# Performance work log

Measured on AMD Instinct MI355X. Metric: run time of the kernel, lower is better.

Reference implementation:

```python
import jax, jax.numpy as jnp
import numpy as np

N, E = 50000, 800000          # nodes, edges (avg degree 16)
NFEAT, NHID, NCLASS = 256, 128, 64
HEADS = 4
P_DROP = 0.5


def setup_inputs() -> dict:
    key = jax.random.key(0)
    ks = jax.random.split(key, 12)

    def w(k, shape, fan_in):
        return jax.random.normal(k, shape, jnp.float32) * (1.0 / np.sqrt(fan_in))

    return {
        "features": jax.random.normal(ks[0], (N, NFEAT), jnp.float32),
        "src": jax.random.randint(ks[1], (E,), 0, N, jnp.int32),
        "dst": jax.random.randint(ks[2], (E,), 0, N, jnp.int32),
        # gc1: nfeat->nhid, 3 layers
        "wqkv1_0": w(ks[3], (3, NFEAT, NHID), NFEAT),
        "wqkv1_r": w(ks[4], (2, 3, NHID, NHID), NHID),
        "wo1": w(ks[5], (3, NHID, NHID), NHID),
        # gc2: nhid->nclass, 3 layers
        "wqkv2_0": w(ks[6], (3, NHID, NCLASS), NHID),
        "wqkv2_r": w(ks[7], (2, 3, NCLASS, NCLASS), NCLASS),
        "wo2": w(ks[8], (3, NCLASS, NCLASS), NCLASS),
        # gc3: nhid->nclass, 3 layers
        "wqkv3_0": w(ks[9], (3, NHID, NCLASS), NHID),
        "wqkv3_r": w(ks[10], (2, 3, NCLASS, NCLASS), NCLASS),
        "wo3": w(ks[11], (3, NCLASS, NCLASS), NCLASS),
    }


def _l2norm(x):
    # F.normalize(x): L2 along dim 1, eps=1e-12
    n = jnp.sqrt(jnp.sum(x * x, axis=1, keepdims=True))
    return x / jnp.maximum(n, 1e-12)


def _graph_transformer(h, src, dst, wqkv0, wqkvr, wo):
    """Stacked graph-transformer layers: gather q[dst]/k[src], edge-softmax per dst, scatter-sum v."""
    n = h.shape[0]
    n_layers = wo.shape[0]
    for l in range(n_layers):  # fixed small structural loop
        w = wqkv0 if l == 0 else wqkvr[l - 1]
        out_dim = w.shape[2]
        dh = out_dim // HEADS
        q = (h @ w[0]).reshape(n, HEADS, dh)
        k = (h @ w[1]).reshape(n, HEADS, dh)
        v = (h @ w[2]).reshape(n, HEADS, dh)
        # per-edge attention scores [E, H]
        s = jnp.einsum('ehd,ehd->eh', q[dst], k[src]) / np.sqrt(dh).astype(np.float32)
        # edge softmax over incoming edges of each dst node
        m = jax.ops.segment_max(s, dst, num_segments=n)
        e = jnp.exp(s - m[dst])
        denom = jax.ops.segment_sum(e, dst, num_segments=n)
        alpha = e / denom[dst]
        agg = jax.ops.segment_sum(alpha[:, :, None] * v[src], dst, num_segments=n)
        h = agg.reshape(n, out_dim) @ wo[l]
        if l < n_layers - 1:
            h = jax.nn.relu(h)
    return h


def reference(features, src, dst, wqkv1_0, wqkv1_r, wo1,
              wqkv2_0, wqkv2_r, wo2, wqkv3_0, wqkv3_r, wo3):
    key = jax.random.key(42)
    kd, ke = jax.random.split(key)

    x = _graph_transformer(features, src, dst, wqkv1_0, wqkv1_r, wo1)
    x = jax.nn.relu(_l2norm(x))
    # dropout (training=True), deterministic key
    keep = jax.random.bernoulli(kd, 1.0 - P_DROP, x.shape)
    x = jnp.where(keep, x / (1.0 - P_DROP), 0.0)

    mu = _l2norm(_graph_transformer(x, src, dst, wqkv2_0, wqkv2_r, wo2))
    logvar = _l2norm(_graph_transformer(x, src, dst, wqkv3_0, wqkv3_r, wo3))

    # reparameterize (training): std = exp(logvar) + 1e-12 (matches source exactly)
    std = jnp.exp(logvar) + 1e-12
    eps = jax.random.normal(ke, std.shape, std.dtype)
    z = eps * std + mu
    return z
```

## Files before the change

kernel.cpp:

```cpp
#include <hip/hip_runtime.h>
#include <stdint.h>
#include <math.h>

#define NN 50000
#define NE 800000
#define NH 4

typedef __attribute__((ext_vector_type(8))) short short8;
typedef __attribute__((ext_vector_type(4))) float floatx4;

__device__ inline float bf2f(uint32_t u16)
{
    return __uint_as_float(u16 << 16);
}
__device__ inline uint16_t f2bf(float f)
{
    uint32_t u = __float_as_uint(f);
    uint32_t r = (u + 0x7fffu + ((u >> 16) & 1u)) >> 16;
    return (uint16_t)r;
}
__device__ inline void unpk2(uint32_t w, float& lo, float& hi)
{
    lo = __uint_as_float(w << 16);
    hi = __uint_as_float(w & 0xffff0000u);
}
__device__ inline void unpk8(uint4 u, float* f)
{
    unpk2(u.x, f[0], f[1]);
    unpk2(u.y, f[2], f[3]);
    unpk2(u.z, f[4], f[5]);
    unpk2(u.w, f[6], f[7]);
}

__device__ inline void dot2bf(float& s, uint32_t a, uint32_t b)
{
    asm("v_dot2_f32_bf16 %0, %1, %2, %0" : "+v"(s) : "v"(a), "v"(b));
}

__device__ inline void wave_lds_sync()
{
    __builtin_amdgcn_wave_barrier();
    asm volatile("s_waitcnt lgkmcnt(0)" ::: "memory");
    __builtin_amdgcn_wave_barrier();
}

__host__ __device__ inline void tf2x32(uint32_t k0, uint32_t k1,
                                       uint32_t x0, uint32_t x1,
                                       uint32_t& o0, uint32_t& o1)
{
    uint32_t ks2 = k0 ^ k1 ^ 0x1BD11BDAu;
    x0 += k0; x1 += k1;
#define TF_R(r) { x0 += x1; x1 = (x1 << (r)) | (x1 >> (32 - (r))); x1 ^= x0; }
    TF_R(13) TF_R(15) TF_R(26) TF_R(6)
    x0 += k1;  x1 += ks2 + 1u;
    TF_R(17) TF_R(29) TF_R(16) TF_R(24)
    x0 += ks2; x1 += k0 + 2u;
    TF_R(13) TF_R(15) TF_R(26) TF_R(6)
    x0 += k0;  x1 += k1 + 3u;
    TF_R(17) TF_R(29) TF_R(16) TF_R(24)
    x0 += k1;  x1 += ks2 + 4u;
    TF_R(13) TF_R(15) TF_R(26) TF_R(6)
    x0 += ks2; x1 += k0 + 5u;
#undef TF_R
    o0 = x0; o1 = x1;
}

__device__ inline uint32_t jax_bits32(uint32_t k0, uint32_t k1, uint32_t idx)
{
    uint32_t a, b;
    tf2x32(k0, k1, 0u, idx, a, b);
    return a ^ b;
}

__device__ inline float jax_u01(uint32_t bits)
{
    return __uint_as_float((bits >> 9) | 0x3f800000u) - 1.0f;
}

__device__ inline float erfinv_f(float x)
{
    float w = -log1pf(-x * x);
    float p;
    if (w < 5.0f) {
        w = w - 2.5f;
        p = 2.81022636e-08f;
        p = fmaf(p, w, 3.43273939e-07f);
        p = fmaf(p, w, -3.5233877e-06f);
        p = fmaf(p, w, -4.39150654e-06f);
        p = fmaf(p, w, 0.00021858087f);
        p = fmaf(p, w, -0.00125372503f);
        p = fmaf(p, w, -0.00417768164f);
        p = fmaf(p, w, 0.246640727f);
        p = fmaf(p, w, 1.50140941f);
    } else {
        w = sqrtf(w) - 3.0f;
        p = -0.000200214257f;
        p = fmaf(p, w, 0.000100950558f);
        p = fmaf(p, w, 0.00134934322f);
        p = fmaf(p, w, -0.00367342844f);
        p = fmaf(p, w, 0.00573950773f);
        p = fmaf(p, w, -0.0076224613f);
        p = fmaf(p, w, 0.00943887047f);
        p = fmaf(p, w, 1.00167406f);
        p = fmaf(p, w, 2.83297682f);
    }
    return p * x;
}

__global__ __launch_bounds__(256) void fill_u32_k(uint32_t* p, uint32_t v, int n)
{
    int i = blockIdx.x * blockDim.x + threadIdx.x;
    if (i < n) p[i] = v;
}

struct WSeg { const float* src; int B, K, C, off; };
struct WSegs { WSeg s[18]; };

__global__ __launch_bounds__(256) void wconv_k(WSegs segs, uint16_t* __restrict__ Wt)
{
    WSeg sg = segs.s[blockIdx.y];
    int n = sg.B * sg.K * sg.C;
    int i = blockIdx.x * 256 + threadIdx.x;
    if (i >= n) return;
    int kc = sg.K * sg.C;
    int b = i / kc;
    int rr = i - b * kc;
    int k = rr / sg.C;
    int c = rr - k * sg.C;
    Wt[(size_t)sg.off + (size_t)(b * sg.C + c) * sg.K + k] = f2bf(sg.src[i]);
}

__global__ __launch_bounds__(256) void hist_k(const int* __restrict__ dst, int* __restrict__ deg)
{
    int e = blockIdx.x * blockDim.x + threadIdx.x;
    if (e < NE) atomicAdd(&deg[dst[e]], 1);
}

#define SCAN_CHUNK 1024
#define SCAN_NBLK  ((NN + SCAN_CHUNK - 1) / SCAN_CHUNK)

__global__ __launch_bounds__(256) void scan1_k(const int* __restrict__ deg,
                                               int* __restrict__ rowptr,
                                               int* __restrict__ bsums)
{
    __shared__ int lds[256];
    int b = blockIdx.x, t = threadIdx.x;
    int base = b * SCAN_CHUNK + t * 4;
    int v0 = (base + 0 < NN) ? deg[base + 0] : 0;
    int v1 = (base + 1 < NN) ? deg[base + 1] : 0;
    int v2 = (base + 2 < NN) ? deg[base + 2] : 0;
    int v3 = (base + 3 < NN) ? deg[base + 3] : 0;
    int s = v0 + v1 + v2 + v3;
    lds[t] = s;
    __syncthreads();
    for (int off = 1; off < 256; off <<= 1) {
        int x = (t >= off) ? lds[t - off] : 0;
        __syncthreads();
        lds[t] += x;
        __syncthreads();
    }
    int excl = lds[t] - s;
    if (base + 0 < NN) rowptr[base + 0] = excl;
    if (base + 1 < NN) rowptr[base + 1] = excl + v0;
    if (base + 2 < NN) rowptr[base + 2] = excl + v0 + v1;
    if (base + 3 < NN) rowptr[base + 3] = excl + v0 + v1 + v2;
    if (t == 255) bsums[b] = lds[255];
}

__global__ void scan2_k(int* bsums)
{
    if (threadIdx.x == 0 && blockIdx.x == 0) {
        int run = 0;
        for (int i = 0; i < SCAN_NBLK; i++) { int t = bsums[i]; bsums[i] = run; run += t; }
    }
}

__global__ __launch_bounds__(256) void scan3_k(int* __restrict__ rowptr,
                                               const int* __restrict__ bsums,
                                               int* __restrict__ cursor)
{
    int i = blockIdx.x * blockDim.x + threadIdx.x;
    if (i < NN) {
        int r = rowptr[i] + bsums[i / SCAN_CHUNK];
        rowptr[i] = r;
        cursor[i] = r;
    }
    if (i == 0) rowptr[NN] = NE;
}

__global__ __launch_bounds__(256) void csr_scatter_k(const int* __restrict__ src,
                                                     const int* __restrict__ dst,
                                                     int* __restrict__ cursor,
                                                     int* __restrict__ esrc)
{
    int e = blockIdx.x * blockDim.x + threadIdx.x;
    if (e >= NE) return;
    int d = dst[e];
    int pos = atomicAdd(&cursor[d], 1);
    esrc[pos] = src[e];
}

struct GArg { const void* A; const uint16_t* W; uint16_t* C; };
struct GArgs2 { GArg a[2]; };

template<int K, int CH, bool AF32>
__global__ __launch_bounds__(256) void gemm_mfma_k(GArgs2 gs, int Ntot, int relu)
{
    constexpr int KP = K + 8;
    constexpr int KC = K / 8;
    constexpr int NT = CH / 16;
    constexpr int CHP = CH + 8;
    constexpr int NIT = (2 * CH) / 64;
    static_assert(64 * CHP <= CH * KP, "epilogue scratch must fit in Ws");
    extern __shared__ uint16_t smem[];
    uint16_t* As = smem;
    uint16_t* Ws = smem + 64 * KP;

    const GArg g = gs.a[blockIdx.y];
    const uint16_t* W = g.W;
    uint16_t* C = g.C;

    const int tid = threadIdx.x;
    const int row0 = blockIdx.x * 64;
    const int w  = tid >> 6;
    const int l  = tid & 63;
    const int lm = l & 15;
    const int lq = l >> 4;

    for (int i = tid; i < 64 * KC; i += 256) {
        int r = i / KC, c = i - r * KC;
        int gr = row0 + r; if (gr >= NN) gr = NN - 1;
        if constexpr (AF32) {
            const float* Af = (const float*)g.A + (size_t)gr * K + c * 8;
            float4 f0 = *(const float4*)Af;
            float4 f1 = *(const float4*)(Af + 4);
            uint4 vv;
            vv.x = (uint32_t)f2bf(f0.x) | ((uint32_t)f2bf(f0.y) << 16);
            vv.y = (uint32_t)f2bf(f0.z) | ((uint32_t)f2bf(f0.w) << 16);
            vv.z = (uint32_t)f2bf(f1.x) | ((uint32_t)f2bf(f1.y) << 16);
            vv.w = (uint32_t)f2bf(f1.z) | ((uint32_t)f2bf(f1.w) << 16);
            *(uint4*)(As + r * KP + c * 8) = vv;
        } else {
            uint4 vv = *(const uint4*)((const uint16_t*)g.A + (size_t)gr * K + c * 8);
            *(uint4*)(As + r * KP + c * 8) = vv;
        }
    }

    const uint16_t* a_base = As + (16 * w + lm) * KP + lq * 8;
    const uint16_t* b_base = Ws + lm * KP + lq * 8;
    uint16_t* sc = Ws + w * 16 * CHP;

    const int nchunks = Ntot / CH;
    for (int ch = 0; ch < nchunks; ch++) {
        __syncthreads();
        for (int i = tid; i < CH * KC; i += 256) {
            int r = i / KC, c = i - r * KC;
            uint4 vv = *(const uint4*)(W + (size_t)(ch * CH + r) * K + c * 8);
            *(uint4*)(Ws + r * KP + c * 8) = vv;
        }
        __syncthreads();

        floatx4 acc[NT];
#pragma unroll
        for (int nt = 0; nt < NT; nt++) acc[nt] = (floatx4){0.f, 0.f, 0.f, 0.f};

#pragma unroll
        for (int ks = 0; ks < K / 32; ks++) {
            short8 av = *(const short8*)(a_base + ks * 32);
#pragma unroll
            for (int nt = 0; nt < NT; nt++) {
                short8 bv = *(const short8*)(b_base + nt * 16 * KP + ks * 32);
                acc[nt] = __builtin_amdgcn_mfma_f32_16x16x32_bf16(av, bv, acc[nt], 0, 0, 0);
            }
        }

        __syncthreads();

#pragma unroll
        for (int nt = 0; nt < NT; nt++) {
#pragma unroll
            for (int r = 0; r < 4; r++) {
                float v = acc[nt][r];
                if (relu) v = fmaxf(v, 0.0f);
                sc[(lq * 4 + r) * CHP + nt * 16 + lm] = f2bf(v);
            }
        }
        wave_lds_sync();

        constexpr int GPR = CH / 8;
#pragma unroll
        for (int it = 0; it < NIT; it++) {
            int i = l + it * 64;
            int rr = i / GPR, cc = (i - rr * GPR) * 8;
            int gr = row0 + 16 * w + rr;
            if (gr < NN) {
                uint4 vv = *(const uint4*)(sc + rr * CHP + cc);
                *(uint4*)(C + (size_t)gr * Ntot + ch * CH + cc) = vv;
            }
        }
    }
}

struct F2Arg { const uint16_t* A; const uint16_t* W1; const uint16_t* W2; uint16_t* C; };
struct F2Args2 { F2Arg a[2]; };

template<int K1, int MODE>
__global__ __launch_bounds__(256) void fused2_k(F2Args2 fs, int Ntot2, uint32_t k0, uint32_t k1)
{
    constexpr int N1 = K1;
    constexpr int CH = 64;
    constexpr int KP = K1 + 8;
    constexpr int KC = K1 / 8;
    constexpr int NC1 = N1 / CH;
    constexpr int NT = CH / 16;
    constexpr int CHP = CH + 8;
    extern __shared__ uint16_t smem[];
    uint16_t* As = smem;
    uint16_t* Xs = As + 64 * KP;
    uint16_t* Ws = Xs + 64 * KP;

    const F2Arg g = fs.a[blockIdx.y];
    const int tid = threadIdx.x;
    const int row0 = blockIdx.x * 64;
    const int w  = tid >> 6;
    const int l  = tid & 63;
    const int lm = l & 15;
    const int lq = l >> 4;

    for (int i = tid; i < 64 * KC; i += 256) {
        int r = i / KC, c = i - r * KC;
        int gr = row0 + r; if (gr >= NN) gr = NN - 1;
        *(uint4*)(As + r * KP + c * 8) = *(const uint4*)(g.A + (size_t)gr * K1 + c * 8);
    }

    const uint16_t* a_base = As + (16 * w + lm) * KP + lq * 8;
    const uint16_t* b_base = Ws + lm * KP + lq * 8;

    floatx4 acc1[NC1][NT];
#pragma unroll
    for (int ch = 0; ch < NC1; ch++)
#pragma unroll
        for (int nt = 0; nt < NT; nt++) acc1[ch][nt] = (floatx4){0.f, 0.f, 0.f, 0.f};

#pragma unroll
    for (int ch = 0; ch < NC1; ch++) {
        __syncthreads();
        for (int i = tid; i < CH * KC; i += 256) {
            int r = i / KC, c = i - r * KC;
            *(uint4*)(Ws + r * KP + c * 8) =
                *(const uint4*)(g.W1 + (size_t)(ch * CH + r) * K1 + c * 8);
        }
        __syncthreads();
#pragma unroll
        for (int ks = 0; ks < K1 / 32; ks++) {
            short8 av = *(const short8*)(a_base + ks * 32);
#pragma unroll
            for (int nt = 0; nt < NT; nt++) {
                short8 bv = *(const short8*)(b_base + nt * 16 * KP + ks * 32);
                acc1[ch][nt] = __builtin_amdgcn_mfma_f32_16x16x32_bf16(av, bv, acc1[ch][nt], 0, 0, 0);
            }
        }
    }

    if constexpr (MODE == 0) {
#pragma unroll
        for (int ch = 0; ch < NC1; ch++)
#pragma unroll
            for (int nt = 0; nt < NT; nt++)
#pragma unroll
                for (int r = 0; r < 4; r++) {
                    float v = fmaxf(acc1[ch][nt][r], 0.0f);
                    Xs[(16 * w + lq * 4 + r) * KP + ch * CH + nt * 16 + lm] = f2bf(v);
                }
    } else {
        float ss[4] = {0.f, 0.f, 0.f, 0.f};
#pragma unroll
        for (int ch = 0; ch < NC1; ch++)
#pragma unroll
            for (int nt = 0; nt < NT; nt++)
#pragma unroll
                for (int r = 0; r < 4; r++)
                    ss[r] = fmaf(acc1[ch][nt][r], acc1[ch][nt][r], ss[r]);
#pragma unroll
        for (int r = 0; r < 4; r++) {
#pragma unroll
            for (int m = 1; m <= 8; m <<= 1) ss[r] += __shfl_xor(ss[r], m, 64);
        }
        const int grow = row0 + 16 * w + lq * 4;
#pragma unroll
        for (int r = 0; r < 4; r++) {
            const float d = fmaxf(sqrtf(ss[r]), 1e-12f);
#pragma unroll
            for (int ch = 0; ch < NC1; ch++)
#pragma unroll
                for (int nt = 0; nt < NT; nt++) {
                    float y = fmaxf(acc1[ch][nt][r] / d, 0.0f);
                    int col = ch * CH + nt * 16 + lm;
                    uint32_t idx = (uint32_t)(grow + r) * (uint32_t)N1 + (uint32_t)col;
                    float u = jax_u01(jax_bits32(k0, k1, idx));
                    Xs[(16 * w + lq * 4 + r) * KP + col] = f2bf((u < 0.5f) ? y * 2.0f : 0.0f);
                }
        }
    }
    __syncthreads();

    const uint16_t* a2_base = Xs + (16 * w + lm) * KP + lq * 8;
    uint16_t* sc = As + w * 16 * CHP;
    const int nch2 = Ntot2 / CH;
    for (int ch = 0; ch < nch2; ch++) {
        for (int i = tid; i < CH * KC; i += 256) {
            int r = i / KC, c = i - r * KC;
            *(uint4*)(Ws + r * KP + c * 8) =
                *(const uint4*)(g.W2 + (size_t)(ch * CH + r) * N1 + c * 8);
        }
        __syncthreads();

        floatx4 acc[NT];
#pragma unroll
        for (int nt = 0; nt < NT; nt++) acc[nt] = (floatx4){0.f, 0.f, 0.f, 0.f};
#pragma unroll
        for (int ks = 0; ks < N1 / 32; ks++) {
            short8 av = *(const short8*)(a2_base + ks * 32);
#pragma unroll
            for (int nt = 0; nt < NT; nt++) {
                short8 bv = *(const short8*)(b_base + nt * 16 * KP + ks * 32);
                acc[nt] = __builtin_amdgcn_mfma_f32_16x16x32_bf16(av, bv, acc[nt], 0, 0, 0);
            }
        }

#pragma unroll
        for (int nt = 0; nt < NT; nt++)
#pragma unroll
            for (int r = 0; r < 4; r++)
                sc[(lq * 4 + r) * CHP + nt * 16 + lm] = f2bf(acc[nt][r]);
        wave_lds_sync();

        constexpr int GPR = CH / 8;
#pragma unroll
        for (int it = 0; it < 2; it++) {
            int i = l + it * 64;
            int rr = i / GPR, cc = (i - rr * GPR) * 8;
            int gr = row0 + 16 * w + rr;
            if (gr < NN)
                *(uint4*)(g.C + (size_t)gr * Ntot2 + ch * CH + cc) = *(const uint4*)(sc + rr * CHP + cc);
        }
        __syncthreads();
    }
}

__global__ __launch_bounds__(256) void final_gemm_k(const uint16_t* __restrict__ Amu,
                                                    const uint16_t* __restrict__ Alv,
                                                    const uint16_t* __restrict__ Wmu,
                                                    const uint16_t* __restrict__ Wlv,
                                                    float* __restrict__ out,
                                                    uint32_t k0, uint32_t k1)
{
    constexpr int K = 64, KP = K + 8, KC = K / 8, NT = 4;
    __shared__ uint16_t As[2][64 * KP];
    __shared__ uint16_t Ws[128 * KP];

    const int tid = threadIdx.x;
    const int row0 = blockIdx.x * 64;
    const int w  = tid >> 6;
    const int l  = tid & 63;
    const int lm = l & 15;
    const int lq = l >> 4;

    for (int i = tid; i < 64 * KC; i += 256) {
        int r = i / KC, c = i - r * KC;
        int gr = row0 + r; if (gr >= NN) gr = NN - 1;
        *(uint4*)(&As[0][r * KP + c * 8]) = *(const uint4*)(Amu + (size_t)gr * K + c * 8);
        *(uint4*)(&As[1][r * KP + c * 8]) = *(const uint4*)(Alv + (size_t)gr * K + c * 8);
    }
    for (int i = tid; i < 128 * KC; i += 256) {
        int r = i / KC, c = i - r * KC;
        uint4 v = (r < 64) ? *(const uint4*)(Wmu + (size_t)r * K + c * 8)
                           : *(const uint4*)(Wlv + (size_t)(r - 64) * K + c * 8);
        *(uint4*)(&Ws[r * KP + c * 8]) = v;
    }
    __syncthreads();

    const uint16_t* amu = &As[0][(16 * w + lm) * KP + lq * 8];
    const uint16_t* alv = &As[1][(16 * w + lm) * KP + lq * 8];
    const uint16_t* bmu = &Ws[lm * KP + lq * 8];
    const uint16_t* blv = &Ws[(64 + lm) * KP + lq * 8];

    floatx4 amu_acc[NT], alv_acc[NT];
#pragma unroll
    for (int nt = 0; nt < NT; nt++) {
        amu_acc[nt] = (floatx4){0.f, 0.f, 0.f, 0.f};
        alv_acc[nt] = (floatx4){0.f, 0.f, 0.f, 0.f};
    }
#pragma unroll
    for (int ks = 0; ks < K / 32; ks++) {
        short8 avm = *(const short8*)(amu + ks * 32);
        short8 avl = *(const short8*)(alv + ks * 32);
#pragma unroll
        for (int nt = 0; nt < NT; nt++) {
            short8 bvm = *(const short8*)(bmu + nt * 16 * KP + ks * 32);
            short8 bvl = *(const short8*)(blv + nt * 16 * KP + ks * 32);
            amu_acc[nt] = __builtin_amdgcn_mfma_f32_16x16x32_bf16(avm, bvm, amu_acc[nt], 0, 0, 0);
            alv_acc[nt] = __builtin_amdgcn_mfma_f32_16x16x32_bf16(avl, bvl, alv_acc[nt], 0, 0, 0);
        }
    }

    float smu[4] = {0.f, 0.f, 0.f, 0.f}, slv[4] = {0.f, 0.f, 0.f, 0.f};
#pragma unroll
    for (int nt = 0; nt < NT; nt++)
#pragma unroll
        for (int r = 0; r < 4; r++) {
            smu[r] = fmaf(amu_acc[nt][r], amu_acc[nt][r], smu[r]);
            slv[r] = fmaf(alv_acc[nt][r], alv_acc[nt][r], slv[r]);
        }
#pragma unroll
    for (int r = 0; r < 4; r++) {
#pragma unroll
        for (int m = 1; m <= 8; m <<= 1) {
            smu[r] += __shfl_xor(smu[r], m, 64);
            slv[r] += __shfl_xor(slv[r], m, 64);
        }
    }

    const float LO = -0.99999994f;
    const int grow = row0 + 16 * w + lq * 4;
#pragma unroll
    for (int r = 0; r < 4; r++) {
        const float dmu = fmaxf(sqrtf(smu[r]), 1e-12f);
        const float dlv = fmaxf(sqrtf(slv[r]), 1e-12f);
        const int gr = grow + r;
#pragma unroll
        for (int nt = 0; nt < NT; nt++) {
            float mu = amu_acc[nt][r] / dmu;
            float lv = alv_acc[nt][r] / dlv;
            uint32_t idx = (uint32_t)gr * 64u + (uint32_t)(nt * 16 + lm);
            float u01 = jax_u01(jax_bits32(k0, k1, idx));
            float u = fmaxf(LO, fmaf(u01, 2.0f, LO));
            float eps = 1.41421354f * erfinv_f(u);
            float stdv = expf(lv) + 1e-12f;
            if (gr < NN) out[idx] = fmaf(eps, stdv, mu);
        }
    }
}

struct AArg { const uint16_t* qkv; uint16_t* agg; };
struct AArgs2 { AArg a[2]; };

template<int DH>
__global__ __launch_bounds__(128) void attn_dual_k(AArgs2 as,
                                                   const int* __restrict__ rowptr,
                                                   const int* __restrict__ esrc,
                                                   float scale2, int str)
{
    constexpr int OD  = NH * DH;
    constexpr int QU  = DH / 8;
    constexpr int CAP = 64;
    constexpr int NP  = CAP / 16;
    constexpr int FV  = OD / 16;
    constexpr int VW  = FV / 2;

    __shared__ float s_sc[2][CAP][4];
    __shared__ int   s_off[2][CAP];

    const uint16_t* qkv = as.a[blockIdx.y].qkv;
    uint16_t* agg       = as.a[blockIdx.y].agg;

    const int wv   = threadIdx.x >> 6;
    const int lane = threadIdx.x & 63;
    const int n    = blockIdx.x * 2 + wv;
    const int h1   = lane & 3;
    const int e    = lane >> 2;
    const int g    = lane >> 4;
    const int dl   = lane & 15;
    const int h2   = dl >> 2;

    uint32_t qw[DH / 2];
    {
        const uint4* q4 = (const uint4*)(qkv + (size_t)n * str + h1 * DH);
#pragma unroll
        for (int i = 0; i < QU; i++) {
            uint4 u = q4[i];
            qw[i * 4 + 0] = u.x; qw[i * 4 + 1] = u.y;
            qw[i * 4 + 2] = u.z; qw[i * 4 + 3] = u.w;
        }
    }

    const int j0 = rowptr[n], j1 = rowptr[n + 1];

    float m = -INFINITY, l = 0.0f;
    float acc[FV];
#pragma unroll
    for (int i = 0; i < FV; i++) acc[i] = 0.0f;

    const int voff = 2 * OD + dl * FV;

    for (int c0 = j0; c0 < j1; c0 += CAP) {
        const int cn = min(j1 - c0, CAP);

        if (lane < cn) s_off[wv][lane] = esrc[c0 + lane] * str;
        wave_lds_sync();

        uint32_t vpre[4][VW];
#pragma unroll
        for (int t = 0; t < 4; t++) {
            const int j  = 4 * t + g;
            const int js = min(j, cn - 1);
            const uint16_t* vp = qkv + s_off[wv][js] + voff;
            if constexpr (VW == 4) {
                uint4 u = *(const uint4*)vp;
                vpre[t][0] = u.x; vpre[t][1] = u.y; vpre[t][2] = u.z; vpre[t][3] = u.w;
            } else {
                uint2 u = *(const uint2*)vp;
                vpre[t][0] = u.x; vpre[t][1] = u.y;
            }
        }

        float p[NP];
        float lm = -INFINITY;
#pragma unroll
        for (int t = 0; t < NP; t++) {
            const int j = e + 16 * t;
            float s = -INFINITY;
            if (j < cn) {
                const uint4* kp = (const uint4*)(qkv + s_off[wv][j] + OD + h1 * DH);
                float a0 = 0.0f, a1 = 0.0f;
#pragma unroll
                for (int i = 0; i < QU; i++) {
                    uint4 u = kp[i];
                    dot2bf(a0, qw[i * 4 + 0], u.x);
                    dot2bf(a1, qw[i * 4 + 1], u.y);
                    dot2bf(a0, qw[i * 4 + 2], u.z);
                    dot2bf(a1, qw[i * 4 + 3], u.w);
                }
                s = (a0 + a1) * scale2;
            }
            p[t] = s;
            lm = fmaxf(lm, s);
        }
#pragma unroll
        for (int msk = 4; msk <= 32; msk <<= 1) lm = fmaxf(lm, __shfl_xor(lm, msk, 64));
        const float mn = fmaxf(m, lm);
        const float corr = exp2f(m - mn);
        m = mn;

        float ls = 0.0f;
#pragma unroll
        for (int t = 0; t < NP; t++) {
            const int j = e + 16 * t;
            float pe = 0.0f;
            if (j < cn) {
                pe = exp2f(p[t] - mn);
                s_sc[wv][j][h1] = pe;
            }
            ls += pe;
        }
#pragma unroll
        for (int msk = 4; msk <= 32; msk <<= 1) ls += __shfl_xor(ls, msk, 64);
        l = l * corr + ls;
        wave_lds_sync();

        const float c2 = __shfl(corr, h2, 64);
#pragma unroll
        for (int i = 0; i < FV; i++) acc[i] *= c2;

#pragma unroll
        for (int t = 0; t < 4; t++) {
            const int j  = 4 * t + g;
            const int js = min(j, cn - 1);
            const float av = s_sc[wv][js][h2];
            const float alpha = (j < cn) ? av : 0.0f;
#pragma unroll
            for (int i = 0; i < VW; i++) {
                float lo, hi;
                unpk2(vpre[t][i], lo, hi);
                acc[2 * i + 0] = fmaf(alpha, lo, acc[2 * i + 0]);
                acc[2 * i + 1] = fmaf(alpha, hi, acc[2 * i + 1]);
            }
        }

        for (int jb = 16; jb < cn; jb += 4) {
            const int j = jb + g;
            if (j < cn) {
                const float alpha = s_sc[wv][j][h2];
                const uint16_t* vp = qkv + s_off[wv][j] + voff;
                if constexpr (FV == 8) {
                    uint4 u = *(const uint4*)vp;
                    float vf[8];
                    unpk8(u, vf);
#pragma unroll
                    for (int i = 0; i < 8; i++) acc[i] = fmaf(alpha, vf[i], acc[i]);
                } else {
                    uint2 u = *(const uint2*)vp;
                    float f0, f1, f2v, f3v;
                    unpk2(u.x, f0, f1);
                    unpk2(u.y, f2v, f3v);
                    acc[0] = fmaf(alpha, f0,  acc[0]);
                    acc[1] = fmaf(alpha, f1,  acc[1]);
                    acc[2] = fmaf(alpha, f2v, acc[2]);
                    acc[3] = fmaf(alpha, f3v, acc[3]);
                }
            }
        }
        wave_lds_sync();
    }

    const float lh = __shfl(l, h2, 64);
    const float inv = (lh > 0.0f) ? 1.0f / lh : 0.0f;
#pragma unroll
    for (int i = 0; i < FV; i++) {
        acc[i] += __shfl_xor(acc[i], 16, 64);
        acc[i] += __shfl_xor(acc[i], 32, 64);
    }
    if (g == 0) {
        uint16_t* op = agg + (size_t)n * OD + dl * FV;
        uint32_t wword[FV / 2];
#pragma unroll
        for (int i = 0; i < FV / 2; i++)
            wword[i] = (uint32_t)f2bf(acc[2 * i] * inv) | ((uint32_t)f2bf(acc[2 * i + 1] * inv) << 16);
        if constexpr (FV == 8) {
            *(uint4*)op = make_uint4(wword[0], wword[1], wword[2], wword[3]);
        } else {
            *(uint2*)op = make_uint2(wword[0], wword[1]);
        }
    }
}

extern "C" void kernel_launch(void* const* d_in, const int* in_sizes, int n_in,
                              void* d_out, int out_size, void* d_ws, size_t ws_size,
                              hipStream_t stream)
{
    const float* feat    = (const float*)d_in[0];
    const int*   src     = (const int*)d_in[1];
    const int*   dst     = (const int*)d_in[2];
    const float* wqkv1_0 = (const float*)d_in[3];
    const float* wqkv1_r = (const float*)d_in[4];
    const float* wo1     = (const float*)d_in[5];
    const float* wqkv2_0 = (const float*)d_in[6];
    const float* wqkv2_r = (const float*)d_in[7];
    const float* wo2     = (const float*)d_in[8];
    const float* wqkv3_0 = (const float*)d_in[9];
    const float* wqkv3_r = (const float*)d_in[10];
    const float* wo3     = (const float*)d_in[11];
    float* out = (float*)d_out;

    char* wp = (char*)d_ws;
    auto alloc = [&](size_t bytes) { char* p = wp; wp += (bytes + 255) & ~(size_t)255; return p; };

    WSegs segs;
    int offs[18];
    int acc_off = 0;
    auto seg = [&](int i, const float* p, int Bc, int Kc, int Cc) {
        segs.s[i].src = p; segs.s[i].B = Bc; segs.s[i].K = Kc; segs.s[i].C = Cc;
        segs.s[i].off = acc_off; offs[i] = acc_off; acc_off += Bc * Kc * Cc;
    };
    seg(0,  wqkv1_0,                 3, 256, 128);
    seg(1,  wqkv1_r,                 3, 128, 128);
    seg(2,  wqkv1_r + 3 * 128 * 128, 3, 128, 128);
    seg(3,  wo1,                     1, 128, 128);
    seg(4,  wo1 + 128 * 128,         1, 128, 128);
    seg(5,  wo1 + 2 * 128 * 128,     1, 128, 128);
    seg(6,  wqkv2_0,                 3, 128, 64);
    seg(7,  wqkv3_0,                 3, 128, 64);
    seg(8,  wqkv2_r,                 3, 64, 64);
    seg(9,  wqkv3_r,                 3, 64, 64);
    seg(10, wqkv2_r + 3 * 64 * 64,   3, 64, 64);
    seg(11, wqkv3_r + 3 * 64 * 64,   3, 64, 64);
    seg(12, wo2,                     1, 64, 64);
    seg(13, wo2 + 64 * 64,           1, 64, 64);
    seg(14, wo2 + 2 * 64 * 64,       1, 64, 64);
    seg(15, wo3,                     1, 64, 64);
    seg(16, wo3 + 64 * 64,           1, 64, 64);
    seg(17, wo3 + 2 * 64 * 64,       1, 64, 64);

    uint16_t* Wt     = (uint16_t*)alloc((size_t)acc_off * 2);
    uint16_t* qkvL   = (uint16_t*)alloc((size_t)NN * 384 * 2);
    uint16_t* agg128 = (uint16_t*)alloc((size_t)NN * 128 * 2);
    uint16_t* qkv_mu = (uint16_t*)alloc((size_t)NN * 192 * 2);
    uint16_t* qkv_lv = (uint16_t*)alloc((size_t)NN * 192 * 2);
    uint16_t* agg_mu = (uint16_t*)alloc((size_t)NN * 64 * 2);
    uint16_t* agg_lv = (uint16_t*)alloc((size_t)NN * 64 * 2);
    int* rowptr = (int*)alloc((size_t)(NN + 1) * 4);
    int* cursor = (int*)alloc((size_t)NN * 4);
    int* bsums  = (int*)alloc((size_t)SCAN_NBLK * 4);
    int* esrc   = (int*)alloc((size_t)NE * 4);

    wconv_k<<<dim3(384, 18), 256, 0, stream>>>(segs, Wt);

    fill_u32_k<<<(NN + 255) / 256, 256, 0, stream>>>((uint32_t*)cursor, 0u, NN);
    hist_k<<<(NE + 255) / 256, 256, 0, stream>>>(dst, cursor);
    scan1_k<<<SCAN_NBLK, 256, 0, stream>>>(cursor, rowptr, bsums);
    scan2_k<<<1, 64, 0, stream>>>(bsums);
    scan3_k<<<(NN + 255) / 256, 256, 0, stream>>>(rowptr, bsums, cursor);
    csr_scatter_k<<<(NE + 255) / 256, 256, 0, stream>>>(src, dst, cursor, esrc);

    uint32_t kd0, kd1, ke0, ke1;
    tf2x32(0u, 42u, 0u, 0u, kd0, kd1);
    tf2x32(0u, 42u, 0u, 1u, ke0, ke1);

    const int GX = (NN + 63) / 64;
    const float LOG2E = 1.4426950408889634f;
    const float sc32 = LOG2E / sqrtf(32.0f);
    const float sc16 = 0.25f * LOG2E;

    auto g1 = [&](GArg a) { GArgs2 g; g.a[0] = a; g.a[1] = a; return g; };
    auto a1 = [&](AArg a) { AArgs2 r; r.a[0] = a; r.a[1] = a; return r; };
    auto a2 = [&](AArg a0, AArg b0) { AArgs2 r; r.a[0] = a0; r.a[1] = b0; return r; };
    auto f1 = [&](F2Arg a) { F2Args2 r; r.a[0] = a; r.a[1] = a; return r; };
    auto f2 = [&](F2Arg a0, F2Arg b0) { F2Args2 r; r.a[0] = a0; r.a[1] = b0; return r; };

    const size_t L256_32 = (size_t)(64 + 32) * (256 + 8) * 2;
    const size_t LF128   = (size_t)192 * (128 + 8) * 2;
    const size_t LF64    = (size_t)192 * (64 + 8) * 2;

    gemm_mfma_k<256, 32, true><<<dim3(GX, 1), 256, L256_32, stream>>>(
        g1({feat, Wt + offs[0], qkvL}), 384, 0);
    attn_dual_k<32><<<dim3(NN / 2, 1), 128, 0, stream>>>(a1({qkvL, agg128}), rowptr, esrc, sc32, 384);

    fused2_k<128, 0><<<dim3(GX, 1), 256, LF128, stream>>>(
        f1({agg128, Wt + offs[3], Wt + offs[1], qkvL}), 384, 0u, 0u);
    attn_dual_k<32><<<dim3(NN / 2, 1), 128, 0, stream>>>(a1({qkvL, agg128}), rowptr, esrc, sc32, 384);

    fused2_k<128, 0><<<dim3(GX, 1), 256, LF128, stream>>>(
        f1({agg128, Wt + offs[4], Wt + offs[2], qkvL}), 384, 0u, 0u);
    attn_dual_k<32><<<dim3(NN / 2, 1), 128, 0, stream>>>(a1({qkvL, agg128}), rowptr, esrc, sc32, 384);

    fused2_k<128, 1><<<dim3(GX, 1), 256, LF128, stream>>>(
        f1({agg128, Wt + offs[5], Wt + offs[6], qkvL}), 384, kd0, kd1);

    attn_dual_k<16><<<dim3(NN / 2, 2), 128, 0, stream>>>(
        a2({qkvL, agg_mu}, {qkvL + 192, agg_lv}), rowptr, esrc, sc16, 384);

    fused2_k<64, 0><<<dim3(GX, 2), 256, LF64, stream>>>(
        f2({agg_mu, Wt + offs[12], Wt + offs[8],  qkv_mu},
           {agg_lv, Wt + offs[15], Wt + offs[9],  qkv_lv}), 192, 0u, 0u);
    attn_dual_k<16><<<dim3(NN / 2, 2), 128, 0, stream>>>(
        a2({qkv_mu, agg_mu}, {qkv_lv, agg_lv}), rowptr, esrc, sc16, 192);

    fused2_k<64, 0><<<dim3(GX, 2), 256, LF64, stream>>>(
        f2({agg_mu, Wt + offs[13], Wt + offs[10], qkv_mu},
           {agg_lv, Wt + offs[16], Wt + offs[11], qkv_lv}), 192, 0u, 0u);
    attn_dual_k<16><<<dim3(NN / 2, 2), 128, 0, stream>>>(
        a2({qkv_mu, agg_mu}, {qkv_lv, agg_lv}), rowptr, esrc, sc16, 192);

    final_gemm_k<<<dim3(GX, 1), 256, 0, stream>>>(
        agg_mu, agg_lv, Wt + offs[14], Wt + offs[17], out, ke0, ke1);
}
```

Before: 796.5 us.

## Split first QKV GEMM across grid.y and pair key loads in attention

The first-layer QKV projection now launches three blocks per row tile along grid.y, each computing one 128-column slice with 64-wide chunks instead of one block looping over all 384 columns. This raises parallelism but makes each block re-read and re-convert its fp32 feature tile, tripling A traffic. The attention score loop now processes two neighbor keys per iteration, issuing both key loads before the dot products to expose more memory-level parallelism, at the cost of more registers.

```diff
diff --git a/kernel.cpp b/kernel.cpp
--- a/kernel.cpp
+++ b/kernel.cpp
@@ -201,10 +201,10 @@
 }
 
 struct GArg { const void* A; const uint16_t* W; uint16_t* C; };
-struct GArgs2 { GArg a[2]; };
+struct GArg3 { GArg a[3]; };
 
 template<int K, int CH, bool AF32>
-__global__ __launch_bounds__(256) void gemm_mfma_k(GArgs2 gs, int Ntot, int relu)
+__global__ __launch_bounds__(256) void gemm_mfma_k(GArg3 gs, int Ntot, int ncols, int relu)
 {
     constexpr int KP = K + 8;
     constexpr int KC = K / 8;
@@ -250,7 +250,7 @@
     const uint16_t* b_base = Ws + lm * KP + lq * 8;
     uint16_t* sc = Ws + w * 16 * CHP;
 
-    const int nchunks = Ntot / CH;
+    const int nchunks = ncols / CH;
     for (int ch = 0; ch < nchunks; ch++) {
         __syncthreads();
         for (int i = tid; i < CH * KC; i += 256) {
@@ -616,25 +616,48 @@
 
         float p[NP];
         float lm = -INFINITY;
-#pragma unroll
-        for (int t = 0; t < NP; t++) {
-            const int j = e + 16 * t;
-            float s = -INFINITY;
-            if (j < cn) {
-                const uint4* kp = (const uint4*)(qkv + s_off[wv][j] + OD + h1 * DH);
+        const int npv = (cn + 15) >> 4;
+#pragma unroll
+        for (int tt = 0; tt < NP; tt += 2) {
+            float sA = -INFINITY, sB = -INFINITY;
+            if (tt < npv) {
+                const int jA = e + 16 * tt;
+                const int jB = jA + 16;
+                const bool hasB = (tt + 1 < npv);
+                uint4 ka[QU], kb[QU];
+                {
+                    const uint4* kp = (const uint4*)(qkv + s_off[wv][min(jA, cn - 1)] + OD + h1 * DH);
+#pragma unroll
+                    for (int i = 0; i < QU; i++) ka[i] = kp[i];
+                }
+                if (hasB) {
+                    const uint4* kp = (const uint4*)(qkv + s_off[wv][min(jB, cn - 1)] + OD + h1 * DH);
+#pragma unroll
+                    for (int i = 0; i < QU; i++) kb[i] = kp[i];
+                }
                 float a0 = 0.0f, a1 = 0.0f;
 #pragma unroll
                 for (int i = 0; i < QU; i++) {
-                    uint4 u = kp[i];
-                    dot2bf(a0, qw[i * 4 + 0], u.x);
-                    dot2bf(a1, qw[i * 4 + 1], u.y);
-                    dot2bf(a0, qw[i * 4 + 2], u.z);
-                    dot2bf(a1, qw[i * 4 + 3], u.w);
+                    dot2bf(a0, qw[i * 4 + 0], ka[i].x);
+                    dot2bf(a1, qw[i * 4 + 1], ka[i].y);
+                    dot2bf(a0, qw[i * 4 + 2], ka[i].z);
+                    dot2bf(a1, qw[i * 4 + 3], ka[i].w);
                 }
-                s = (a0 + a1) * scale2;
-            }
-            p[t] = s;
-            lm = fmaxf(lm, s);
+                if (jA < cn) sA = (a0 + a1) * scale2;
+                if (hasB) {
+                    float b0 = 0.0f, b1 = 0.0f;
+#pragma unroll
+                    for (int i = 0; i < QU; i++) {
+                        dot2bf(b0, qw[i * 4 + 0], kb[i].x);
+                        dot2bf(b1, qw[i * 4 + 1], kb[i].y);
+                        dot2bf(b0, qw[i * 4 + 2], kb[i].z);
+                        dot2bf(b1, qw[i * 4 + 3], kb[i].w);
+                    }
+                    if (jB < cn) sB = (b0 + b1) * scale2;
+                }
+            }
+            p[tt] = sA; p[tt + 1] = sB;
+            lm = fmaxf(lm, fmaxf(sA, sB));
         }
 #pragma unroll
         for (int msk = 4; msk <= 32; msk <<= 1) lm = fmaxf(lm, __shfl_xor(lm, msk, 64));
@@ -801,18 +824,19 @@
     const float sc32 = LOG2E / sqrtf(32.0f);
     const float sc16 = 0.25f * LOG2E;
 
-    auto g1 = [&](GArg a) { GArgs2 g; g.a[0] = a; g.a[1] = a; return g; };
     auto a1 = [&](AArg a) { AArgs2 r; r.a[0] = a; r.a[1] = a; return r; };
     auto a2 = [&](AArg a0, AArg b0) { AArgs2 r; r.a[0] = a0; r.a[1] = b0; return r; };
     auto f1 = [&](F2Arg a) { F2Args2 r; r.a[0] = a; r.a[1] = a; return r; };
     auto f2 = [&](F2Arg a0, F2Arg b0) { F2Args2 r; r.a[0] = a0; r.a[1] = b0; return r; };
 
-    const size_t L256_32 = (size_t)(64 + 32) * (256 + 8) * 2;
+    const size_t L256_64 = (size_t)(64 + 64) * (256 + 8) * 2;
     const size_t LF128   = (size_t)192 * (128 + 8) * 2;
     const size_t LF64    = (size_t)192 * (64 + 8) * 2;
 
-    gemm_mfma_k<256, 32, true><<<dim3(GX, 1), 256, L256_32, stream>>>(
-        g1({feat, Wt + offs[0], qkvL}), 384, 0);
+    GArg3 gf;
+    for (int y = 0; y < 3; y++)
+        gf.a[y] = GArg{feat, Wt + offs[0] + (size_t)y * 128 * 256, qkvL + y * 128};
+    gemm_mfma_k<256, 64, true><<<dim3(GX, 3), 256, L256_64, stream>>>(gf, 384, 128, 0);
     attn_dual_k<32><<<dim3(NN / 2, 1), 128, 0, stream>>>(a1({qkvL, agg128}), rowptr, esrc, sc32, 384);
 
     fused2_k<128, 0><<<dim3(GX, 1), 256, LF128, stream>>>(
```

Measured after the change: 808.8 us. Within noise of the previous version (+1.5%).

## Split first QKV GEMM across grid.y and alias LDS buffers in fused GEMM

Applied to the files above, without the earlier changes.

The first feature GEMM is split three ways along grid.y, one launch slice per Q/K/V column block of 128, and uses 64-column chunks instead of 32. This gives each block less serial work and the launch more blocks. In fused2_k, the activation and intermediate share a single LDS buffer, and the store scratch moves into the weight buffer, shrinking shared memory so more blocks can be resident per CU. The cost is extra barriers per chunk and repeated reads/conversions of the fp32 feature rows across the three grid slices.

```diff
diff --git a/kernel.cpp b/kernel.cpp
--- a/kernel.cpp
+++ b/kernel.cpp
@@ -201,10 +201,10 @@
 }
 
 struct GArg { const void* A; const uint16_t* W; uint16_t* C; };
-struct GArgs2 { GArg a[2]; };
+struct GArg3 { GArg a[3]; };
 
 template<int K, int CH, bool AF32>
-__global__ __launch_bounds__(256) void gemm_mfma_k(GArgs2 gs, int Ntot, int relu)
+__global__ __launch_bounds__(256) void gemm_mfma_k(GArg3 gs, int Ntot, int ncols, int relu)
 {
     constexpr int KP = K + 8;
     constexpr int KC = K / 8;
@@ -250,7 +250,7 @@
     const uint16_t* b_base = Ws + lm * KP + lq * 8;
     uint16_t* sc = Ws + w * 16 * CHP;
 
-    const int nchunks = Ntot / CH;
+    const int nchunks = ncols / CH;
     for (int ch = 0; ch < nchunks; ch++) {
         __syncthreads();
         for (int i = tid; i < CH * KC; i += 256) {
@@ -314,10 +314,10 @@
     constexpr int NC1 = N1 / CH;
     constexpr int NT = CH / 16;
     constexpr int CHP = CH + 8;
+    static_assert(64 * CHP <= CH * KP, "store scratch must fit in Ws");
     extern __shared__ uint16_t smem[];
-    uint16_t* As = smem;
-    uint16_t* Xs = As + 64 * KP;
-    uint16_t* Ws = Xs + 64 * KP;
+    uint16_t* AXs = smem;
+    uint16_t* Ws  = AXs + 64 * KP;
 
     const F2Arg g = fs.a[blockIdx.y];
     const int tid = threadIdx.x;
@@ -330,10 +330,10 @@
     for (int i = tid; i < 64 * KC; i += 256) {
         int r = i / KC, c = i - r * KC;
         int gr = row0 + r; if (gr >= NN) gr = NN - 1;
-        *(uint4*)(As + r * KP + c * 8) = *(const uint4*)(g.A + (size_t)gr * K1 + c * 8);
-    }
-
-    const uint16_t* a_base = As + (16 * w + lm) * KP + lq * 8;
+        *(uint4*)(AXs + r * KP + c * 8) = *(const uint4*)(g.A + (size_t)gr * K1 + c * 8);
+    }
+
+    const uint16_t* a_base = AXs + (16 * w + lm) * KP + lq * 8;
     const uint16_t* b_base = Ws + lm * KP + lq * 8;
 
     floatx4 acc1[NC1][NT];
@@ -362,6 +362,7 @@
         }
     }
 
+    wave_lds_sync();
     if constexpr (MODE == 0) {
 #pragma unroll
         for (int ch = 0; ch < NC1; ch++)
@@ -370,7 +371,7 @@
 #pragma unroll
                 for (int r = 0; r < 4; r++) {
                     float v = fmaxf(acc1[ch][nt][r], 0.0f);
-                    Xs[(16 * w + lq * 4 + r) * KP + ch * CH + nt * 16 + lm] = f2bf(v);
+                    AXs[(16 * w + lq * 4 + r) * KP + ch * CH + nt * 16 + lm] = f2bf(v);
                 }
     } else {
         float ss[4] = {0.f, 0.f, 0.f, 0.f};
@@ -398,16 +399,15 @@
                     int col = ch * CH + nt * 16 + lm;
                     uint32_t idx = (uint32_t)(grow + r) * (uint32_t)N1 + (uint32_t)col;
                     float u = jax_u01(jax_bits32(k0, k1, idx));
-                    Xs[(16 * w + lq * 4 + r) * KP + col] = f2bf((u < 0.5f) ? y * 2.0f : 0.0f);
+                    AXs[(16 * w + lq * 4 + r) * KP + col] = f2bf((u < 0.5f) ? y * 2.0f : 0.0f);
                 }
         }
     }
-    __syncthreads();
-
-    const uint16_t* a2_base = Xs + (16 * w + lm) * KP + lq * 8;
-    uint16_t* sc = As + w * 16 * CHP;
+
+    uint16_t* sc = Ws + w * 16 * CHP;
     const int nch2 = Ntot2 / CH;
     for (int ch = 0; ch < nch2; ch++) {
+        __syncthreads();
         for (int i = tid; i < CH * KC; i += 256) {
             int r = i / KC, c = i - r * KC;
             *(uint4*)(Ws + r * KP + c * 8) =
@@ -420,13 +420,15 @@
         for (int nt = 0; nt < NT; nt++) acc[nt] = (floatx4){0.f, 0.f, 0.f, 0.f};
 #pragma unroll
         for (int ks = 0; ks < N1 / 32; ks++) {
-            short8 av = *(const short8*)(a2_base + ks * 32);
+            short8 av = *(const short8*)(a_base + ks * 32);
 #pragma unroll
             for (int nt = 0; nt < NT; nt++) {
                 short8 bv = *(const short8*)(b_base + nt * 16 * KP + ks * 32);
                 acc[nt] = __builtin_amdgcn_mfma_f32_16x16x32_bf16(av, bv, acc[nt], 0, 0, 0);
             }
         }
+
+        __syncthreads();
 
 #pragma unroll
         for (int nt = 0; nt < NT; nt++)
@@ -444,7 +446,6 @@
             if (gr < NN)
                 *(uint4*)(g.C + (size_t)gr * Ntot2 + ch * CH + cc) = *(const uint4*)(sc + rr * CHP + cc);
         }
-        __syncthreads();
     }
 }
 
@@ -801,18 +802,19 @@
     const float sc32 = LOG2E / sqrtf(32.0f);
     const float sc16 = 0.25f * LOG2E;
 
-    auto g1 = [&](GArg a) { GArgs2 g; g.a[0] = a; g.a[1] = a; return g; };
     auto a1 = [&](AArg a) { AArgs2 r; r.a[0] = a; r.a[1] = a; return r; };
     auto a2 = [&](AArg a0, AArg b0) { AArgs2 r; r.a[0] = a0; r.a[1] = b0; return r; };
     auto f1 = [&](F2Arg a) { F2Args2 r; r.a[0] = a; r.a[1] = a; return r; };
     auto f2 = [&](F2Arg a0, F2Arg b0) { F2Args2 r; r.a[0] = a0; r.a[1] = b0; return r; };
 
-    const size_t L256_32 = (size_t)(64 + 32) * (256 + 8) * 2;
-    const size_t LF128   = (size_t)192 * (128 + 8) * 2;
-    const size_t LF64    = (size_t)192 * (64 + 8) * 2;
-
-    gemm_mfma_k<256, 32, true><<<dim3(GX, 1), 256, L256_32, stream>>>(
-        g1({feat, Wt + offs[0], qkvL}), 384, 0);
+    const size_t L256_64 = (size_t)(64 + 64) * (256 + 8) * 2;
+    const size_t LF128   = (size_t)(64 + 64) * (128 + 8) * 2;
+    const size_t LF64    = (size_t)(64 + 64) * (64 + 8) * 2;
+
+    GArg3 gf;
+    for (int y = 0; y < 3; y++)
+        gf.a[y] = GArg{feat, Wt + offs[0] + (size_t)y * 128 * 256, qkvL + y * 128};
+    gemm_mfma_k<256, 64, true><<<dim3(GX, 3), 256, L256_64, stream>>>(gf, 384, 128, 0);
     attn_dual_k<32><<<dim3(NN / 2, 1), 128, 0, stream>>>(a1({qkvL, agg128}), rowptr, esrc, sc32, 384);
 
     fused2_k<128, 0><<<dim3(GX, 1), 256, LF128, stream>>>(
```

Measured after the change: 759.8 us (median of 3 runs). -4.6%, faster.
